# Kernel tuning notes

Measured on AMD Instinct MI355X. Metric: run time of the kernel, lower is better.

Reference implementation:

```python
import jax, jax.numpy as jnp
import numpy as np

LN_EPS = 1e-5
EPS = 1e-8
MESH_LR = 1.0
MESH_ITERS = 4
SH_ITERS = 5
SA_ITERS = 3


def build_grid(res):
    ranges = [np.linspace(0.0, 1.0, num=r) for r in res]
    g = np.stack(np.meshgrid(*ranges, indexing='ij'), axis=-1)
    g = g.reshape(res[0], res[1], -1)[None]
    return jnp.asarray(np.concatenate([g, 1.0 - g], axis=-1).astype(np.float32))  # [1,H,W,4]


def layer_norm(x, w, b):
    m = jnp.mean(x, axis=-1, keepdims=True)
    v = jnp.var(x, axis=-1, keepdims=True)
    return (x - m) * jax.lax.rsqrt(v + LN_EPS) * w + b


def l2norm(x):
    n = jnp.linalg.norm(x, axis=-1, keepdims=True)
    return x / jnp.maximum(n, 1e-12)  # matches F.normalize eps


def conv_relu(x, w, b, stride):
    y = jax.lax.conv_general_dilated(x, w, (stride, stride), [(2, 2), (2, 2)],
                                     dimension_numbers=('NCHW', 'OIHW', 'NCHW'))
    return jax.nn.relu(y + b[None, :, None, None])


def sinkhorn(C, a, b, u=None, v=None, n_iters=SH_ITERS):
    # log-domain Sinkhorn; C: [B,N,S] cost, a: [B,N], b: [B,S] marginals
    p = -C
    log_a, log_b = jnp.log(a), jnp.log(b)
    if u is None:
        u = jnp.zeros_like(a)
    if v is None:
        v = jnp.zeros_like(b)
    for _ in range(n_iters):
        u = log_a - jax.nn.logsumexp(p + v[:, None, :], axis=2)
        v = log_b - jax.nn.logsumexp(p + u[:, :, None], axis=1)
    pi = jnp.exp(p + u[:, :, None] + v[:, None, :])
    return pi, u, v


def minimize_entropy_of_sinkhorn(C0, a, b, mesh_lr=MESH_LR, n_mesh_iters=MESH_ITERS):
    # gradient descent on the cost matrix to minimize entropy of the transport plan
    def ent(C, u, v):
        pi, u2, v2 = sinkhorn(C, a, b, u=u, v=v)
        e = jnp.mean(-jnp.sum(pi * jnp.log(pi + EPS), axis=(1, 2)))
        return e, (u2, v2)

    grad_fn = jax.grad(ent, has_aux=True)
    u, v = jnp.zeros_like(a), jnp.zeros_like(b)
    C = C0
    for _ in range(n_mesh_iters):
        g, (u, v) = grad_fn(C, u, v)
        C = C - mesh_lr * g
    return C, u, v


def gru_cell(x, h, wih, whh, bih, bhh):
    gi = x @ wih.T + bih
    gh = h @ whh.T + bhh
    ir, iz, inn = jnp.split(gi, 3, axis=-1)
    hr, hz, hn = jnp.split(gh, 3, axis=-1)
    r = jax.nn.sigmoid(ir + hr)
    z = jax.nn.sigmoid(iz + hz)
    n = jnp.tanh(inn + r * hn)
    return (1.0 - z) * n + z * h


def setup_inputs() -> dict:
    key = jax.random.key(0)
    ks = iter(jax.random.split(key, 48))

    def nrm(shape, fan_in):
        return jax.random.normal(next(ks), shape, jnp.float32) / np.sqrt(fan_in).astype(np.float32)

    B, d, S, HID = 16, 64, 8, 128
    z = lambda *s: jnp.zeros(s, jnp.float32)
    o = lambda *s: jnp.ones(s, jnp.float32)
    inp = {
        'image': jax.random.normal(next(ks), (B, 3, 128, 128), jnp.float32),
        'slots_noise': jax.random.normal(next(ks), (B, S, d), jnp.float32),
        'conv1_w': nrm((64, 3, 5, 5), 75), 'conv1_b': z(64),
        'conv2_w': nrm((64, 64, 5, 5), 1600), 'conv2_b': z(64),
        'conv3_w': nrm((64, 64, 5, 5), 1600), 'conv3_b': z(64),
        'conv4_w': nrm((64, 64, 5, 5), 1600), 'conv4_b': z(64),
        'pos_w': nrm((d, 4), 4), 'pos_b': z(d),
        'mlp1_w': nrm((d, d), d), 'mlp1_b': z(d),
        'mlp2_w': nrm((d, d), d), 'mlp2_b': z(d),
        'ln_in_w': o(d), 'ln_in_b': z(d),
        'wk': nrm((d, d), d), 'wv': nrm((d, d), d), 'wq': nrm((d, d), d),
        'mwi_w': nrm((1, d), d), 'mwi_b': z(1),
        'mws_w': nrm((1, d), d), 'mws_b': z(1),
        'ln_sl_w': o(d), 'ln_sl_b': z(d),
        'gru_wih': nrm((3 * d, d), d), 'gru_whh': nrm((3 * d, d), d),
        'gru_bih': z(3 * d), 'gru_bhh': z(3 * d),
        'ln_ff_w': o(d), 'ln_ff_b': z(d),
        'fc1_w': nrm((HID, d), d), 'fc1_b': z(HID),
        'fc2_w': nrm((d, HID), HID), 'fc2_b': z(d),
        'slots_mu': nrm((1, 1, d), d),
        'slots_sigma': jax.random.uniform(next(ks), (1, 1, d), jnp.float32),
        'num_slots': 8,
    }
    return inp


def reference(image, slots_noise, conv1_w, conv1_b, conv2_w, conv2_b, conv3_w, conv3_b,
              conv4_w, conv4_b, pos_w, pos_b, mlp1_w, mlp1_b, mlp2_w, mlp2_b,
              ln_in_w, ln_in_b, wk, wv, wq, mwi_w, mwi_b, mws_w, mws_b,
              ln_sl_w, ln_sl_b, gru_wih, gru_whh, gru_bih, gru_bhh,
              ln_ff_w, ln_ff_b, fc1_w, fc1_b, fc2_w, fc2_b,
              slots_mu, slots_sigma, num_slots):
    B = image.shape[0]
    d = slots_mu.shape[-1]
    # --- CNN encoder (strided_convs=True => latent 32x32) ---
    x = conv_relu(image, conv1_w, conv1_b, 1)
    x = conv_relu(x, conv2_w, conv2_b, 2)
    x = conv_relu(x, conv3_w, conv3_b, 2)
    x = conv_relu(x, conv4_w, conv4_b, 1)          # [B,64,32,32]
    x = x.transpose(0, 2, 3, 1)                    # [B,32,32,64]
    grid = build_grid((32, 32))                    # [1,32,32,4]
    x = x + (grid @ pos_w.T + pos_b)               # soft position embed
    feat = x.reshape(B, -1, d)                     # [B,1024,64]
    # --- pre-slot-attention MLP ---
    feat = jax.nn.relu(feat @ mlp1_w.T + mlp1_b) @ mlp2_w.T + mlp2_b
    # --- slot attention with MESH-Sinkhorn ---
    n_s = num_slots
    slots = slots_mu + (jnp.abs(slots_sigma) + EPS) * slots_noise  # Normal rsample
    inp = layer_norm(feat, ln_in_w, ln_in_b)
    k = inp @ wk.T
    v = inp @ wv.T
    a = jax.nn.softmax((inp @ mwi_w.T + mwi_b).squeeze(-1), axis=-1) * n_s  # [B,N]
    kn = l2norm(k)
    attn = None
    for _ in range(SA_ITERS):
        slots_prev = slots
        s = layer_norm(slots, ln_sl_w, ln_sl_b)
        bm = jax.nn.softmax((s @ mws_w.T + mws_b).squeeze(-1), axis=-1) * n_s  # [B,S]
        q = s @ wq.T
        C = 1.0 - jnp.einsum('bnd,bsd->bns', kn, l2norm(q))  # cosine distance
        C, p, qq = minimize_entropy_of_sinkhorn(C, a, bm)
        pi, _, _ = sinkhorn(C, a, bm, u=p, v=qq)
        attn = pi.transpose(0, 2, 1)                         # [B,S,N]
        updates = jnp.einsum('bsn,bnd->bsd', attn, v)
        slots = gru_cell(updates.reshape(-1, d), slots_prev.reshape(-1, d),
                         gru_wih, gru_whh, gru_bih, gru_bhh).reshape(B, n_s, d)
        h = layer_norm(slots, ln_ff_w, ln_ff_b)
        slots = slots + (jax.nn.relu(h @ fc1_w.T + fc1_b) @ fc2_w.T + fc2_b)
    return slots, attn
```

## Files before the change

### kernel.cpp

```cpp
#include <hip/hip_runtime.h>
#include <hip/hip_bf16.h>


#define LN_EPS 1e-5f
#define SEPS 1e-8f
#define LN8 2.0794415416798357f

__device__ inline float ldf(float x) { return x; }
__device__ inline float ldf(__hip_bfloat16 x) { return __bfloat162float(x); }
__device__ inline void stf(float* p, float v) { *p = v; }
__device__ inline void stf(__hip_bfloat16* p, float v) { *p = __float2bfloat16(v); }

__device__ inline float wmaxall(float v) {
#pragma unroll
  for (int o = 32; o; o >>= 1) v = fmaxf(v, __shfl_down(v, o));
  return __shfl(v, 0);
}
__device__ inline float wsumall(float v) {
#pragma unroll
  for (int o = 32; o; o >>= 1) v += __shfl_down(v, o);
  return __shfl(v, 0);
}
__device__ inline int wsumi(int v) {
#pragma unroll
  for (int o = 32; o; o >>= 1) v += __shfl_down(v, o);
  return __shfl(v, 0);
}
__device__ inline float fast_sigmoid(float x) { return 1.f / (1.f + __expf(-x)); }
__device__ inline float fast_tanh(float x) { return 1.f - 2.f / (__expf(2.f * x) + 1.f); }

struct CvtArgs {
  const void* src[39];
  long off[40];
};

__global__ __launch_bounds__(256) void convert_kernel(CvtArgs a,
                                                      float* __restrict__ dst, long total) {
  __shared__ int sFlag;
  {
    const unsigned int* img = (const unsigned int*)a.src[0];
    if (threadIdx.x < 64) {
      int cnt = 0;
      for (int i = threadIdx.x; i < 512; i += 64) {
        unsigned lo = img[i] & 0xFFFFu;
        int e = (int)((lo >> 7) & 0xFFu);
        cnt += (e >= 96 && e <= 140) ? 1 : 0;
      }
      cnt = wsumi(cnt);
      if (threadIdx.x == 0) sFlag = (cnt >= 300) ? 1 : 0;
    }
    __syncthreads();
  }
  const int isbf = sFlag;
  for (long g = (long)blockIdx.x * 256 + threadIdx.x; g < total; g += (long)gridDim.x * 256) {
    int lo = 0, hi = 38;
    while (lo < hi) {
      int mid = (lo + hi + 1) >> 1;
      if (a.off[mid] <= g) lo = mid; else hi = mid - 1;
    }
    long li = g - a.off[lo];
    float v;
    if (isbf) v = __bfloat162float(((const __hip_bfloat16*)a.src[lo])[li]);
    else      v = ((const float*)a.src[lo])[li];
    dst[g] = v;
  }
}

struct TwArgs {
  long soff[9]; long doff[9]; int R[9]; int C[9];
};

__global__ __launch_bounds__(256) void transw_kernel(const float* __restrict__ cvt,
                                                     float* __restrict__ tws, TwArgs a) {
  int m = blockIdx.x;
  const float* S = cvt + a.soff[m];
  float* D = tws + a.doff[m];
  int R = a.R[m], C = a.C[m];
  for (int idx = threadIdx.x; idx < R * C; idx += 256) {
    int i = idx / C, j = idx - i * C;
    D[j * R + i] = S[idx];
  }
}

template <int S, typename TIN, typename TOUT>
__global__ __launch_bounds__(256) void conv5x5(
    const TIN* __restrict__ in, const float* __restrict__ wgt,
    const float* __restrict__ bias, TOUT* __restrict__ out,
    int Cin, int H, int W, int Ho, int Wo, int Cout, int tilesX) {
  constexpr int P = 15 * S + 5;
  constexpr int PP = (S == 1) ? 20 : 40;
  constexpr int NCH = (S == 1) ? 2 : 3;
  constexpr int NP = (P * P + 255) / 256;
  __shared__ __align__(16) float patch[P * PP];
  __shared__ float wt16[25 * 16];
  const int b = blockIdx.z;
  const int ocg = blockIdx.y * 16;
  const int ty0 = (blockIdx.x / tilesX) * 16, tx0 = (blockIdx.x % tilesX) * 16;
  const int og = threadIdx.x >> 6;
  const int r = (threadIdx.x >> 2) & 15;
  const int rx = threadIdx.x & 3;
  const int iy0 = ty0 * S - 2, ix0 = tx0 * S - 2;
  const long HW = (long)H * W;

  int toff[NP], soff[NP];
#pragma unroll
  for (int q = 0; q < NP; q++) {
    int idx = threadIdx.x + 256 * q;
    toff[q] = -1;
    soff[q] = -1;
    if (idx < P * P) {
      int py = idx / P, px = idx - py * P;
      int iy = iy0 + py, ix = ix0 + px;
      int pxs = (S == 2) ? (px ^ (((py >> 1) & 1) << 2)) : px;
      toff[q] = py * PP + pxs;
      if (iy >= 0 && iy < H && ix >= 0 && ix < W) soff[q] = iy * W + ix;
    }
  }
  int wsrc[2];
#pragma unroll
  for (int q = 0; q < 2; q++) {
    int idx = threadIdx.x + 256 * q;
    wsrc[q] = (idx < 400) ? (((ocg + (idx & 15)) * Cin) * 25 + (idx >> 4)) : -1;
  }

  float acc[4][4];
#pragma unroll
  for (int p = 0; p < 4; p++)
#pragma unroll
    for (int j = 0; j < 4; j++) acc[p][j] = 0.f;

  float pr[NP], wr[2];
  {
    const TIN* inp = in + (long)b * Cin * HW;
#pragma unroll
    for (int q = 0; q < NP; q++) pr[q] = (soff[q] >= 0) ? ldf(inp[soff[q]]) : 0.f;
#pragma unroll
    for (int q = 0; q < 2; q++) wr[q] = (wsrc[q] >= 0) ? wgt[wsrc[q]] : 0.f;
  }

  for (int ci = 0; ci < Cin; ++ci) {
    __syncthreads();
#pragma unroll
    for (int q = 0; q < NP; q++)
      if (toff[q] >= 0) patch[toff[q]] = pr[q];
#pragma unroll
    for (int q = 0; q < 2; q++) {
      int idx = threadIdx.x + 256 * q;
      if (idx < 400) wt16[idx] = wr[q];
    }
    __syncthreads();
    if (ci + 1 < Cin) {
      const TIN* inp = in + ((long)b * Cin + ci + 1) * HW;
#pragma unroll
      for (int q = 0; q < NP; q++) pr[q] = (soff[q] >= 0) ? ldf(inp[soff[q]]) : 0.f;
#pragma unroll
      for (int q = 0; q < 2; q++)
        if (wsrc[q] >= 0) wr[q] = wgt[wsrc[q] + (ci + 1) * 25];
    }
#pragma unroll
    for (int ky = 0; ky < 5; ky++) {
      float win[4 * NCH];
      const int row = r * S + ky;
      const float* rb = &patch[row * PP];
      if constexpr (S == 2) {
        const int sw = (row >> 1) & 1;
#pragma unroll
        for (int c = 0; c < NCH; c++) {
          const int g = rx * 2 + c;
          float4 t4 = *(const float4*)(rb + ((g ^ sw) << 2));
          win[4 * c + 0] = t4.x;
          win[4 * c + 1] = t4.y;
          win[4 * c + 2] = t4.z;
          win[4 * c + 3] = t4.w;
        }
      } else {
        const float* bp = rb + rx * 4;
#pragma unroll
        for (int c = 0; c < NCH; c++) {
          float4 t4 = *(const float4*)(bp + 4 * c);
          win[4 * c + 0] = t4.x;
          win[4 * c + 1] = t4.y;
          win[4 * c + 2] = t4.z;
          win[4 * c + 3] = t4.w;
        }
      }
#pragma unroll
      for (int kx = 0; kx < 5; kx++) {
        const float4 wv = *(const float4*)&wt16[(ky * 5 + kx) * 16 + og * 4];
#pragma unroll
        for (int p = 0; p < 4; p++) {
          float iv = win[p * S + kx];
          acc[p][0] += iv * wv.x;
          acc[p][1] += iv * wv.y;
          acc[p][2] += iv * wv.z;
          acc[p][3] += iv * wv.w;
        }
      }
    }
  }
  const int oy = ty0 + r, ox0 = tx0 + rx * 4;
#pragma unroll
  for (int j = 0; j < 4; j++) {
    int oc = ocg + og * 4 + j;
    float bs = bias[oc];
    TOUT* op = &out[(((long)b * Cout + oc) * Ho + oy) * Wo + ox0];
#pragma unroll
    for (int p = 0; p < 4; p++) stf(&op[p], fmaxf(acc[p][j] + bs, 0.f));
  }
}

template <int S, typename TIN>
__global__ __launch_bounds__(256) void conv5x5_part(
    const TIN* __restrict__ in, const float* __restrict__ wgt,
    float* __restrict__ pout,
    int Cin, int H, int W, int Ho, int Wo, int Cout, int tilesX) {
  constexpr int P = 15 * S + 5;
  constexpr int PP = (S == 1) ? 20 : 40;
  constexpr int NCH = (S == 1) ? 2 : 3;
  constexpr int NP = (P * P + 255) / 256;
  __shared__ __align__(16) float patch[P * PP];
  __shared__ float wt16[25 * 16];
  const int zz = blockIdx.z;
  const int qh = zz & 3;
  const int b = zz >> 2;
  const int nci = Cin >> 2;
  const int c0 = qh * nci;
  const int ocg = blockIdx.y * 16;
  const int ty0 = (blockIdx.x / tilesX) * 16, tx0 = (blockIdx.x % tilesX) * 16;
  const int og = threadIdx.x >> 6;
  const int r = (threadIdx.x >> 2) & 15;
  const int rx = threadIdx.x & 3;
  const int iy0 = ty0 * S - 2, ix0 = tx0 * S - 2;
  const long HW = (long)H * W;

  int toff[NP], soff[NP];
#pragma unroll
  for (int q = 0; q < NP; q++) {
    int idx = threadIdx.x + 256 * q;
    toff[q] = -1;
    soff[q] = -1;
    if (idx < P * P) {
      int py = idx / P, px = idx - py * P;
      int iy = iy0 + py, ix = ix0 + px;
      int pxs = (S == 2) ? (px ^ (((py >> 1) & 1) << 2)) : px;
      toff[q] = py * PP + pxs;
      if (iy >= 0 && iy < H && ix >= 0 && ix < W) soff[q] = iy * W + ix;
    }
  }
  int wsrc[2];
#pragma unroll
  for (int q = 0; q < 2; q++) {
    int idx = threadIdx.x + 256 * q;
    wsrc[q] = (idx < 400) ? (((ocg + (idx & 15)) * Cin) * 25 + (idx >> 4)) : -1;
  }

  float acc[4][4];
#pragma unroll
  for (int p = 0; p < 4; p++)
#pragma unroll
    for (int j = 0; j < 4; j++) acc[p][j] = 0.f;

  float pr[NP], wr[2];
  {
    const TIN* inp = in + ((long)b * Cin + c0) * HW;
#pragma unroll
    for (int q = 0; q < NP; q++) pr[q] = (soff[q] >= 0) ? ldf(inp[soff[q]]) : 0.f;
#pragma unroll
    for (int q = 0; q < 2; q++) wr[q] = (wsrc[q] >= 0) ? wgt[wsrc[q] + c0 * 25] : 0.f;
  }

  const int cEnd = c0 + nci;
  for (int ci = c0; ci < cEnd; ++ci) {
    __syncthreads();
#pragma unroll
    for (int q = 0; q < NP; q++)
      if (toff[q] >= 0) patch[toff[q]] = pr[q];
#pragma unroll
    for (int q = 0; q < 2; q++) {
      int idx = threadIdx.x + 256 * q;
      if (idx < 400) wt16[idx] = wr[q];
    }
    __syncthreads();
    if (ci + 1 < cEnd) {
      const TIN* inp = in + ((long)b * Cin + ci + 1) * HW;
#pragma unroll
      for (int q = 0; q < NP; q++) pr[q] = (soff[q] >= 0) ? ldf(inp[soff[q]]) : 0.f;
#pragma unroll
      for (int q = 0; q < 2; q++)
        if (wsrc[q] >= 0) wr[q] = wgt[wsrc[q] + (ci + 1) * 25];
    }
#pragma unroll
    for (int ky = 0; ky < 5; ky++) {
      float win[4 * NCH];
      const int row = r * S + ky;
      const float* rb = &patch[row * PP];
      if constexpr (S == 2) {
        const int sw = (row >> 1) & 1;
#pragma unroll
        for (int c = 0; c < NCH; c++) {
          const int g = rx * 2 + c;
          float4 t4 = *(const float4*)(rb + ((g ^ sw) << 2));
          win[4 * c + 0] = t4.x;
          win[4 * c + 1] = t4.y;
          win[4 * c + 2] = t4.z;
          win[4 * c + 3] = t4.w;
        }
      } else {
        const float* bp = rb + rx * 4;
#pragma unroll
        for (int c = 0; c < NCH; c++) {
          float4 t4 = *(const float4*)(bp + 4 * c);
          win[4 * c + 0] = t4.x;
          win[4 * c + 1] = t4.y;
          win[4 * c + 2] = t4.z;
          win[4 * c + 3] = t4.w;
        }
      }
#pragma unroll
      for (int kx = 0; kx < 5; kx++) {
        const float4 wv = *(const float4*)&wt16[(ky * 5 + kx) * 16 + og * 4];
#pragma unroll
        for (int p = 0; p < 4; p++) {
          float iv = win[p * S + kx];
          acc[p][0] += iv * wv.x;
          acc[p][1] += iv * wv.y;
          acc[p][2] += iv * wv.z;
          acc[p][3] += iv * wv.w;
        }
      }
    }
  }
  const int oy = ty0 + r, ox0 = tx0 + rx * 4;
  const long HoWo = (long)Ho * Wo;
#pragma unroll
  for (int j = 0; j < 4; j++) {
    int oc = ocg + og * 4 + j;
    float* op = &pout[((((long)qh * 16 + b) * Cout + oc) * Ho + oy) * Wo + ox0];
    (void)HoWo;
#pragma unroll
    for (int p = 0; p < 4; p++) op[p] = acc[p][j];
  }
}

__global__ __launch_bounds__(256) void fuse4_kernel(
    const float* __restrict__ pin, const float* __restrict__ bias,
    float* __restrict__ outF, int HoWo, int Cout, long qtr) {
  for (long i = (long)blockIdx.x * 256 + threadIdx.x; i < qtr;
       i += (long)gridDim.x * 256) {
    int oc = (int)((i / HoWo) % Cout);
    float v = ((pin[i] + pin[i + qtr]) + pin[i + 2 * qtr]) + pin[i + 3 * qtr];
    outF[i] = fmaxf(v + bias[oc], 0.f);
  }
}

__global__ __launch_bounds__(256) void token_kernel(
    const float* __restrict__ act4, const float* __restrict__ pos_w,
    const float* __restrict__ pos_b,
    const float* __restrict__ mlp1T, const float* __restrict__ mlp1_b,
    const float* __restrict__ mlp2T, const float* __restrict__ mlp2_b,
    const float* __restrict__ lnin_w, const float* __restrict__ lnin_b,
    const float* __restrict__ wkT, const float* __restrict__ wvT,
    const float* __restrict__ mwi_w, const float* __restrict__ mwi_b,
    float* __restrict__ knT_out, float* __restrict__ v_out, float* __restrict__ lg_out) {
  const int wq = threadIdx.x >> 6, i = threadIdx.x & 63;
  const int t = blockIdx.x * 4 + wq;
  const int b = t >> 10, nn = t & 1023;
  const int h = nn >> 5, w = nn & 31;
  __shared__ float sM1[4096], sM2[4096], sWk[4096], sWv[4096];
  __shared__ float f[4][64], h1[4][64], inp[4][64];
  for (int idx = threadIdx.x; idx < 4096; idx += 256) {
    sM1[idx] = mlp1T[idx];
    sM2[idx] = mlp2T[idx];
    sWk[idx] = wkT[idx];
    sWv[idx] = wvT[idx];
  }
  {
    float gh = h * (1.f / 31.f), gw = w * (1.f / 31.f);
    float e = gh * pos_w[i * 4 + 0] + gw * pos_w[i * 4 + 1] +
              (1.f - gh) * pos_w[i * 4 + 2] + (1.f - gw) * pos_w[i * 4 + 3] + pos_b[i];
    f[wq][i] = act4[(((long)b * 64 + i) * 32 + h) * 32 + w] + e;
  }
  __syncthreads();
  float acc = 0.f;
  for (int j = 0; j < 64; j++) acc += f[wq][j] * sM1[j * 64 + i];
  h1[wq][i] = fmaxf(acc + mlp1_b[i], 0.f);
  __syncthreads();
  acc = 0.f;
  for (int j = 0; j < 64; j++) acc += h1[wq][j] * sM2[j * 64 + i];
  float x = acc + mlp2_b[i];
  float m = wsumall(x) * (1.f / 64.f);
  float d0 = x - m;
  float var = wsumall(d0 * d0) * (1.f / 64.f);
  float xin = d0 * rsqrtf(var + LN_EPS) * lnin_w[i] + lnin_b[i];
  inp[wq][i] = xin;
  __syncthreads();
  float kv = 0.f, vv = 0.f;
  for (int j = 0; j < 64; j++) {
    float ij = inp[wq][j];
    kv += ij * sWk[j * 64 + i];
    vv += ij * sWv[j * 64 + i];
  }
  float ss = wsumall(kv * kv);
  knT_out[(long)b * 65536 + i * 1024 + nn] = kv / fmaxf(sqrtf(ss), 1e-12f);
  v_out[(long)t * 64 + i] = vv;
  float lg = wsumall(xin * mwi_w[i]);
  if (i == 0) lg_out[t] = lg + mwi_b[0];
}

__global__ __launch_bounds__(512) void sa_kernel(
    const float* __restrict__ knT_g, const float* __restrict__ v_g,
    const float* __restrict__ la_g, const float* __restrict__ noise,
    const float* __restrict__ mu_w, const float* __restrict__ sg_w,
    const float* __restrict__ lnsl_w, const float* __restrict__ lnsl_b,
    const float* __restrict__ mws_w, const float* __restrict__ mws_b,
    const float* __restrict__ wqT,
    const float* __restrict__ wihT, const float* __restrict__ whhT,
    const float* __restrict__ bih, const float* __restrict__ bhh,
    const float* __restrict__ lnff_w, const float* __restrict__ lnff_b,
    const float* __restrict__ fc1T, const float* __restrict__ fc1_b,
    const float* __restrict__ fc2T, const float* __restrict__ fc2_b,
    float* __restrict__ out) {
  const int b = blockIdx.x, tid = threadIdx.x;
  const int wv = tid >> 6, ln = tid & 63;

  __shared__ float sCt[8192];
  __shared__ float sEc[8192];
  __shared__ float sLa[1024], sELa[1024], sHid[1024];
  __shared__ float sPart[512 * 9];
  __shared__ float sVh[48], sV[8], sEsv[8], sGv[8], sLb[8], sBm[8];
  __shared__ float sC1[8], sEvh[8];
  __shared__ float sSlots[512], sNorm[512], sQn[512], sUpd[512];

  const float* knt = knT_g + (long)b * 65536;
  const float* vf = v_g + (long)b * 65536;
  float sInvH[5][2];
  float gPr[2][8];
  float gInit[2];

  {
    int dd = tid & 63;
    sSlots[tid] = mu_w[dd] + (fabsf(sg_w[dd]) + SEPS) * noise[(long)b * 512 + tid];
  }
  for (int n = tid; n < 1024; n += 512) sLa[n] = la_g[b * 1024 + n];
  __syncthreads();
  {
    float a0 = sLa[tid], a1 = sLa[tid + 512];
    float m0 = wmaxall(fmaxf(a0, a1));
    if (ln == 0) sBm[wv] = m0;
    __syncthreads();
    float M = sBm[0];
#pragma unroll
    for (int s = 1; s < 8; s++) M = fmaxf(M, sBm[s]);
    float e0 = wsumall(__expf(a0 - M) + __expf(a1 - M));
    if (ln == 0) sGv[wv] = e0;
    __syncthreads();
    float SS = 0.f;
#pragma unroll
    for (int s = 0; s < 8; s++) SS += sGv[s];
    float lse = M + __logf(SS);
    float l0 = a0 - lse + LN8, l1 = a1 - lse + LN8;
    sLa[tid] = l0;
    sLa[tid + 512] = l1;
    sELa[tid] = __expf(l0);
    sELa[tid + 512] = __expf(l1);
  }
  __syncthreads();

  for (int it = 0; it < 3; ++it) {
    {
      float x = sSlots[wv * 64 + ln];
      float m = wsumall(x) * (1.f / 64.f);
      float d0 = x - m;
      float var = wsumall(d0 * d0) * (1.f / 64.f);
      float xn = d0 * rsqrtf(var + LN_EPS) * lnsl_w[ln] + lnsl_b[ln];
      sNorm[wv * 64 + ln] = xn;
      float bmv = wsumall(xn * mws_w[ln]);
      if (ln == 0) sBm[wv] = bmv + mws_b[0];
    }
    __syncthreads();
    if (tid == 0) {
      float mx = -1e30f;
      for (int s = 0; s < 8; s++) mx = fmaxf(mx, sBm[s]);
      float ss = 0.f;
      for (int s = 0; s < 8; s++) ss += __expf(sBm[s] - mx);
      float lse = mx + __logf(ss);
      for (int s = 0; s < 8; s++) sLb[s] = sBm[s] - lse + LN8;
    }
    {
      float acc = 0.f;
      for (int j = 0; j < 64; j++) acc += sNorm[wv * 64 + j] * wqT[j * 64 + ln];
      sQn[tid] = acc;
    }
    __syncthreads();
    {
      float qv = sQn[wv * 64 + ln];
      float ss = wsumall(qv * qv);
      sQn[wv * 64 + ln] = qv / fmaxf(sqrtf(ss), 1e-12f);
    }
    if (tid < 8) {
      sV[tid] = 0.f;
      sEsv[tid] = 1.f;
    }
    __syncthreads();

#pragma unroll
    for (int k = 0; k < 2; k++) {
      int n = tid + 512 * k;
      float acc[8];
#pragma unroll
      for (int s = 0; s < 8; s++) acc[s] = 0.f;
      for (int j = 0; j < 64; j++) {
        float kvv = knt[j * 1024 + n];
#pragma unroll
        for (int s = 0; s < 8; s++) acc[s] += kvv * sQn[s * 64 + j];
      }
#pragma unroll
      for (int s = 0; s < 8; s++) {
        float c = 1.f - acc[s];
        sCt[s * 1024 + n] = c;
        sEc[s * 1024 + n] = __expf(-c);
      }
    }
    __syncthreads();

    for (int m = 0; m < 4; m++) {
#pragma unroll
      for (int t = 1; t <= 5; t++) {
        if (t == 1 && tid < 8) sVh[tid] = sV[tid];
        float esv_r[8], part[8];
#pragma unroll
        for (int s = 0; s < 8; s++) { esv_r[s] = sEsv[s]; part[s] = 0.f; }
#pragma unroll
        for (int k = 0; k < 2; k++) {
          int n = tid + 512 * k;
          float ec[8], S = 0.f;
#pragma unroll
          for (int s = 0; s < 8; s++) {
            ec[s] = sEc[s * 1024 + n];
            S += esv_r[s] * ec[s];
          }
          float inv = 1.f / S;
          sInvH[t - 1][k] = inv;
          float w = sELa[n] * inv;
#pragma unroll
          for (int s = 0; s < 8; s++) part[s] += w * ec[s];
        }
#pragma unroll
        for (int s = 0; s < 8; s++) sPart[tid * 9 + s] = part[s];
        __syncthreads();
        {
          int s = wv;
          float acc = 0.f;
#pragma unroll
          for (int q = 0; q < 8; q++) acc += sPart[(ln + 64 * q) * 9 + s];
          acc = wsumall(acc);
          if (ln == 0) {
            float vs = sLb[s] - __logf(acc);
            sV[s] = vs;
            sVh[t * 8 + s] = vs;
            sEsv[s] = __expf(vs);
          }
        }
        __syncthreads();
      }
      {
        float esv_r[8], part[8];
#pragma unroll
        for (int s = 0; s < 8; s++) { esv_r[s] = sEsv[s]; part[s] = 0.f; }
#pragma unroll
        for (int k = 0; k < 2; k++) {
          int n = tid + 512 * k;
          float al = sELa[n] * sInvH[4][k];
          float gul = 0.f;
#pragma unroll
          for (int s = 0; s < 8; s++) {
            float pi = al * esv_r[s] * sEc[s * 1024 + n];
            float gl = -(__logf(pi + SEPS) + pi / (pi + SEPS)) * pi * (1.f / 16.f);
            gPr[k][s] = gl;
            gul += gl;
            part[s] += gl;
          }
          gInit[k] = gul;
        }
#pragma unroll
        for (int s = 0; s < 8; s++) sPart[tid * 9 + s] = part[s];
        __syncthreads();
        {
          int s = wv;
          float acc = 0.f;
#pragma unroll
          for (int q = 0; q < 8; q++) acc += sPart[(ln + 64 * q) * 9 + s];
          acc = wsumall(acc);
          if (ln == 0) {
            sGv[s] = acc;
            sC1[s] = acc * __expf(sVh[40 + s] - sLb[s]);
            sEvh[s] = __expf(sVh[32 + s]);
          }
        }
        __syncthreads();
      }
#pragma unroll
      for (int t = 5; t >= 1; t--) {
        float c1_r[8], evh_r[8], part[8];
#pragma unroll
        for (int s = 0; s < 8; s++) {
          c1_r[s] = sC1[s];
          evh_r[s] = sEvh[s];
          part[s] = 0.f;
        }
#pragma unroll
        for (int k = 0; k < 2; k++) {
          int n = tid + 512 * k;
          float inv = sInvH[t - 1][k];
          float al = sELa[n] * inv;
          float gul = (t == 5) ? gInit[k] : 0.f;
          float ec[8];
#pragma unroll
          for (int s = 0; s < 8; s++) {
            ec[s] = sEc[s * 1024 + n];
            float t2 = al * c1_r[s] * ec[s];
            gPr[k][s] -= t2;
            gul -= t2;
          }
          float bv = gul * inv;
#pragma unroll
          for (int s = 0; s < 8; s++) {
            float pe = bv * ec[s];
            gPr[k][s] -= pe * evh_r[s];
            part[s] += pe;
          }
          if (t == 1) {
#pragma unroll
            for (int s = 0; s < 8; s++) {
              float cn = sCt[s * 1024 + n] + gPr[k][s];
              sCt[s * 1024 + n] = cn;
              sEc[s * 1024 + n] = __expf(-cn);
            }
          }
        }
        if (t > 1) {
#pragma unroll
          for (int s = 0; s < 8; s++) sPart[tid * 9 + s] = part[s];
        }
        if (t == 1 && tid < 8) {
          float vs = sVh[40 + tid];
          sV[tid] = vs;
          sEsv[tid] = __expf(vs);
        }
        __syncthreads();
        if (t > 1) {
          int s = wv;
          float acc = 0.f;
#pragma unroll
          for (int q = 0; q < 8; q++) acc += sPart[(ln + 64 * q) * 9 + s];
          acc = wsumall(acc);
          if (ln == 0) {
            float gn = -sEvh[s] * acc;
            sGv[s] = gn;
            sC1[s] = gn * __expf(sVh[(t - 1) * 8 + s] - sLb[s]);
            sEvh[s] = __expf(sVh[(t - 2) * 8 + s]);
          }
          __syncthreads();
        }
      }
    }

    float invF[2];
    for (int t = 0; t < 5; t++) {
      float esv_r[8], part[8];
#pragma unroll
      for (int s = 0; s < 8; s++) { esv_r[s] = sEsv[s]; part[s] = 0.f; }
#pragma unroll
      for (int k = 0; k < 2; k++) {
        int n = tid + 512 * k;
        float ec[8], S = 0.f;
#pragma unroll
        for (int s = 0; s < 8; s++) {
          ec[s] = sEc[s * 1024 + n];
          S += esv_r[s] * ec[s];
        }
        float inv = 1.f / S;
        invF[k] = inv;
        float w = sELa[n] * inv;
#pragma unroll
        for (int s = 0; s < 8; s++) part[s] += w * ec[s];
      }
#pragma unroll
      for (int s = 0; s < 8; s++) sPart[tid * 9 + s] = part[s];
      __syncthreads();
      {
        int s = wv;
        float acc = 0.f;
#pragma unroll
        for (int q = 0; q < 8; q++) acc += sPart[(ln + 64 * q) * 9 + s];
        acc = wsumall(acc);
        if (ln == 0) {
          float vs = sLb[s] - __logf(acc);
          sV[s] = vs;
          sEsv[s] = __expf(vs);
        }
      }
      __syncthreads();
    }
    {
      float esv_r[8];
#pragma unroll
      for (int s = 0; s < 8; s++) esv_r[s] = sEsv[s];
#pragma unroll
      for (int k = 0; k < 2; k++) {
        int n = tid + 512 * k;
        float al = sELa[n] * invF[k];
#pragma unroll
        for (int s = 0; s < 8; s++)
          sCt[s * 1024 + n] = al * esv_r[s] * sEc[s * 1024 + n];
      }
    }
    __syncthreads();
    if (it == 2) {
      for (int o = tid; o < 8192; o += 512) out[8192 + (long)b * 8192 + o] = sCt[o];
    }
    {
      int s = tid >> 6, dd = tid & 63;
      float acc = 0.f;
      for (int n = 0; n < 1024; n++) acc += sCt[s * 1024 + n] * vf[n * 64 + dd];
      sUpd[tid] = acc;
    }
    __syncthreads();
    float newslot;
    {
      int s = tid >> 6, i = tid & 63;
      const float* x = &sUpd[s * 64];
      const float* h = &sSlots[s * 64];
      float gir = 0, giz = 0, gin = 0, ghr = 0, ghz = 0, ghn = 0;
      for (int j = 0; j < 64; j++) {
        float xv = x[j], hv = h[j];
        gir += xv * wihT[j * 192 + i];
        giz += xv * wihT[j * 192 + 64 + i];
        gin += xv * wihT[j * 192 + 128 + i];
        ghr += hv * whhT[j * 192 + i];
        ghz += hv * whhT[j * 192 + 64 + i];
        ghn += hv * whhT[j * 192 + 128 + i];
      }
      gir += bih[i]; giz += bih[64 + i]; gin += bih[128 + i];
      ghr += bhh[i]; ghz += bhh[64 + i]; ghn += bhh[128 + i];
      float r = fast_sigmoid(gir + ghr);
      float z = fast_sigmoid(giz + ghz);
      float nn = fast_tanh(gin + r * ghn);
      newslot = (1.f - z) * nn + z * h[i];
    }
    __syncthreads();
    sSlots[tid] = newslot;
    __syncthreads();
    {
      float x = sSlots[wv * 64 + ln];
      float m = wsumall(x) * (1.f / 64.f);
      float d0 = x - m;
      float var = wsumall(d0 * d0) * (1.f / 64.f);
      sNorm[wv * 64 + ln] = d0 * rsqrtf(var + LN_EPS) * lnff_w[ln] + lnff_b[ln];
    }
    __syncthreads();
    for (int o = tid; o < 1024; o += 512) {
      int s = o >> 7, k2 = o & 127;
      float acc = 0.f;
      for (int j = 0; j < 64; j++) acc += sNorm[s * 64 + j] * fc1T[j * 128 + k2];
      sHid[o] = fmaxf(acc + fc1_b[k2], 0.f);
    }
    __syncthreads();
    {
      int s = tid >> 6, i = tid & 63;
      float acc = 0.f;
      for (int j = 0; j < 128; j++) acc += sHid[s * 128 + j] * fc2T[j * 64 + i];
      newslot = sSlots[tid] + acc + fc2_b[i];
    }
    __syncthreads();
    sSlots[tid] = newslot;
    __syncthreads();
  }
  out[(long)b * 512 + tid] = sSlots[tid];
}

extern "C" void kernel_launch(void* const* d_in, const int* in_sizes, int n_in,
                              void* d_out, int out_size, void* d_ws, size_t ws_size,
                              hipStream_t stream) {
  (void)n_in; (void)out_size; (void)ws_size;
  char* ws = (char*)d_ws;
  float* cvt  = (float*)ws;
  float* lgts = (float*)(ws + 5570560ull);
  __hip_bfloat16* act1 = (__hip_bfloat16*)(ws + 5636096ull);
  __hip_bfloat16* act2 = (__hip_bfloat16*)(ws + 39190528ull);
  float* act3 = (float*)(ws + 5636096ull);
  float* act4 = (float*)(ws + 9830400ull);
  float* knT  = (float*)(ws + 14024704ull);
  float* vf   = (float*)(ws + 18219008ull);
  float* parts = (float*)(ws + 22413312ull);
  float* tws  = (float*)(ws + 47583232ull);

  CvtArgs ca;
  long total = 0;
  for (int i = 0; i < 39; i++) { ca.src[i] = d_in[i]; ca.off[i] = total; total += in_sizes[i]; }
  ca.off[39] = total;

  convert_kernel<<<1024, 256, 0, stream>>>(ca, cvt, total);

#define ARR(i) (cvt + ca.off[i])
  TwArgs ta;
  {
    const int src[9] = {12, 14, 18, 19, 20, 27, 28, 33, 35};
    const int R[9] = {64, 64, 64, 64, 64, 192, 192, 128, 64};
    const int C[9] = {64, 64, 64, 64, 64, 64, 64, 64, 128};
    long d = 0;
    for (int m2 = 0; m2 < 9; m2++) {
      ta.soff[m2] = ca.off[src[m2]];
      ta.doff[m2] = d;
      ta.R[m2] = R[m2];
      ta.C[m2] = C[m2];
      d += (long)R[m2] * C[m2];
    }
  }
  transw_kernel<<<9, 256, 0, stream>>>(cvt, tws, ta);
  float* mlp1T = tws + 0,     *mlp2T = tws + 4096,  *wkT = tws + 8192, *wvT = tws + 12288;
  float* wqT   = tws + 16384, *wihT  = tws + 20480, *whhT = tws + 32768;
  float* fc1T  = tws + 45056, *fc2T  = tws + 53248;

  const float* image = ARR(0);
  const float* noise = ARR(1);

  conv5x5<1, float, __hip_bfloat16><<<dim3(64, 4, 16), 256, 0, stream>>>(
      image, ARR(2), ARR(3), act1, 3, 128, 128, 128, 128, 64, 8);
  conv5x5<2, __hip_bfloat16, __hip_bfloat16><<<dim3(16, 4, 16), 256, 0, stream>>>(
      act1, ARR(4), ARR(5), act2, 64, 128, 128, 64, 64, 64, 4);
  conv5x5_part<2, __hip_bfloat16><<<dim3(4, 4, 64), 256, 0, stream>>>(
      act2, ARR(6), parts, 64, 64, 64, 32, 32, 64, 2);
  fuse4_kernel<<<1024, 256, 0, stream>>>(parts, ARR(7), act3, 1024, 64,
                                         16L * 64 * 1024);
  conv5x5_part<1, float><<<dim3(4, 4, 64), 256, 0, stream>>>(
      act3, ARR(8), parts, 64, 32, 32, 32, 32, 64, 2);
  fuse4_kernel<<<1024, 256, 0, stream>>>(parts, ARR(9), act4, 1024, 64,
                                         16L * 64 * 1024);

  token_kernel<<<4096, 256, 0, stream>>>(act4, ARR(10), ARR(11),
                                         mlp1T, ARR(13), mlp2T, ARR(15),
                                         ARR(16), ARR(17), wkT, wvT, ARR(21), ARR(22),
                                         knT, vf, lgts);

  sa_kernel<<<16, 512, 0, stream>>>(knT, vf, lgts, noise, ARR(37), ARR(38),
                                    ARR(25), ARR(26), ARR(23), ARR(24), wqT,
                                    wihT, whhT, ARR(29), ARR(30),
                                    ARR(31), ARR(32), fc1T, ARR(34), fc2T, ARR(36),
                                    (float*)d_out);
#undef ARR
}
```

Before: 863.9 us.

## Halve conv_part tile height for more blocks and fuse final split-K reduction into token kernel

The split-K conv kernel now uses 8-row output tiles with 2 output channels per thread group instead of 16 rows and 4 channels. This doubles the grid size and lowers per-thread register use, giving more parallelism for the small late convolutions. The last fuse4 reduction and ReLU pass is removed: the token kernel sums the four partial buffers and applies bias and ReLU itself, which saves one launch and one full activation round trip. In exchange each thread does less arithmetic per shared-memory load, and the patch loads overlap more between neighbouring tiles.

```diff
diff --git a/kernel.cpp b/kernel.cpp
--- a/kernel.cpp
+++ b/kernel.cpp
@@ -214,11 +214,12 @@
     const TIN* __restrict__ in, const float* __restrict__ wgt,
     float* __restrict__ pout,
     int Cin, int H, int W, int Ho, int Wo, int Cout, int tilesX) {
-  constexpr int P = 15 * S + 5;
+  constexpr int PR = 7 * S + 5;
+  constexpr int PC = 15 * S + 5;
   constexpr int PP = (S == 1) ? 20 : 40;
   constexpr int NCH = (S == 1) ? 2 : 3;
-  constexpr int NP = (P * P + 255) / 256;
-  __shared__ __align__(16) float patch[P * PP];
+  constexpr int NP = (PR * PC + 255) / 256;
+  __shared__ __align__(16) float patch[PR * PP];
   __shared__ float wt16[25 * 16];
   const int zz = blockIdx.z;
   const int qh = zz & 3;
@@ -226,9 +227,9 @@
   const int nci = Cin >> 2;
   const int c0 = qh * nci;
   const int ocg = blockIdx.y * 16;
-  const int ty0 = (blockIdx.x / tilesX) * 16, tx0 = (blockIdx.x % tilesX) * 16;
-  const int og = threadIdx.x >> 6;
-  const int r = (threadIdx.x >> 2) & 15;
+  const int ty0 = (blockIdx.x / tilesX) * 8, tx0 = (blockIdx.x % tilesX) * 16;
+  const int og = threadIdx.x >> 5;
+  const int r = (threadIdx.x >> 2) & 7;
   const int rx = threadIdx.x & 3;
   const int iy0 = ty0 * S - 2, ix0 = tx0 * S - 2;
   const long HW = (long)H * W;
@@ -239,8 +240,8 @@
     int idx = threadIdx.x + 256 * q;
     toff[q] = -1;
     soff[q] = -1;
-    if (idx < P * P) {
-      int py = idx / P, px = idx - py * P;
+    if (idx < PR * PC) {
+      int py = idx / PC, px = idx - py * PC;
       int iy = iy0 + py, ix = ix0 + px;
       int pxs = (S == 2) ? (px ^ (((py >> 1) & 1) << 2)) : px;
       toff[q] = py * PP + pxs;
@@ -254,11 +255,12 @@
     wsrc[q] = (idx < 400) ? (((ocg + (idx & 15)) * Cin) * 25 + (idx >> 4)) : -1;
   }
 
-  float acc[4][4];
-#pragma unroll
-  for (int p = 0; p < 4; p++)
-#pragma unroll
-    for (int j = 0; j < 4; j++) acc[p][j] = 0.f;
+  float acc[4][2];
+#pragma unroll
+  for (int p = 0; p < 4; p++) {
+    acc[p][0] = 0.f;
+    acc[p][1] = 0.f;
+  }
 
   float pr[NP], wr[2];
   {
@@ -318,25 +320,22 @@
       }
 #pragma unroll
       for (int kx = 0; kx < 5; kx++) {
-        const float4 wv = *(const float4*)&wt16[(ky * 5 + kx) * 16 + og * 4];
+        const float* wp = &wt16[(ky * 5 + kx) * 16 + og * 2];
+        float w0 = wp[0], w1 = wp[1];
 #pragma unroll
         for (int p = 0; p < 4; p++) {
           float iv = win[p * S + kx];
-          acc[p][0] += iv * wv.x;
-          acc[p][1] += iv * wv.y;
-          acc[p][2] += iv * wv.z;
-          acc[p][3] += iv * wv.w;
+          acc[p][0] += iv * w0;
+          acc[p][1] += iv * w1;
         }
       }
     }
   }
   const int oy = ty0 + r, ox0 = tx0 + rx * 4;
-  const long HoWo = (long)Ho * Wo;
-#pragma unroll
-  for (int j = 0; j < 4; j++) {
-    int oc = ocg + og * 4 + j;
+#pragma unroll
+  for (int j = 0; j < 2; j++) {
+    int oc = ocg + og * 2 + j;
     float* op = &pout[((((long)qh * 16 + b) * Cout + oc) * Ho + oy) * Wo + ox0];
-    (void)HoWo;
 #pragma unroll
     for (int p = 0; p < 4; p++) op[p] = acc[p][j];
   }
@@ -354,8 +353,8 @@
 }
 
 __global__ __launch_bounds__(256) void token_kernel(
-    const float* __restrict__ act4, const float* __restrict__ pos_w,
-    const float* __restrict__ pos_b,
+    const float* __restrict__ parts, const float* __restrict__ cb4,
+    const float* __restrict__ pos_w, const float* __restrict__ pos_b,
     const float* __restrict__ mlp1T, const float* __restrict__ mlp1_b,
     const float* __restrict__ mlp2T, const float* __restrict__ mlp2_b,
     const float* __restrict__ lnin_w, const float* __restrict__ lnin_b,
@@ -378,7 +377,10 @@
     float gh = h * (1.f / 31.f), gw = w * (1.f / 31.f);
     float e = gh * pos_w[i * 4 + 0] + gw * pos_w[i * 4 + 1] +
               (1.f - gh) * pos_w[i * 4 + 2] + (1.f - gw) * pos_w[i * 4 + 3] + pos_b[i];
-    f[wq][i] = act4[(((long)b * 64 + i) * 32 + h) * 32 + w] + e;
+    const long base = ((long)b * 64 + i) * 1024 + nn;
+    const long q = 16L * 64 * 1024;
+    float v = ((parts[base] + parts[base + q]) + parts[base + 2 * q]) + parts[base + 3 * q];
+    f[wq][i] = fmaxf(v + cb4[i], 0.f) + e;
   }
   __syncthreads();
   float acc = 0.f;
@@ -789,7 +791,6 @@
   __hip_bfloat16* act1 = (__hip_bfloat16*)(ws + 5636096ull);
   __hip_bfloat16* act2 = (__hip_bfloat16*)(ws + 39190528ull);
   float* act3 = (float*)(ws + 5636096ull);
-  float* act4 = (float*)(ws + 9830400ull);
   float* knT  = (float*)(ws + 14024704ull);
   float* vf   = (float*)(ws + 18219008ull);
   float* parts = (float*)(ws + 22413312ull);
@@ -829,16 +830,14 @@
       image, ARR(2), ARR(3), act1, 3, 128, 128, 128, 128, 64, 8);
   conv5x5<2, __hip_bfloat16, __hip_bfloat16><<<dim3(16, 4, 16), 256, 0, stream>>>(
       act1, ARR(4), ARR(5), act2, 64, 128, 128, 64, 64, 64, 4);
-  conv5x5_part<2, __hip_bfloat16><<<dim3(4, 4, 64), 256, 0, stream>>>(
+  conv5x5_part<2, __hip_bfloat16><<<dim3(8, 4, 64), 256, 0, stream>>>(
       act2, ARR(6), parts, 64, 64, 64, 32, 32, 64, 2);
   fuse4_kernel<<<1024, 256, 0, stream>>>(parts, ARR(7), act3, 1024, 64,
                                          16L * 64 * 1024);
-  conv5x5_part<1, float><<<dim3(4, 4, 64), 256, 0, stream>>>(
+  conv5x5_part<1, float><<<dim3(8, 4, 64), 256, 0, stream>>>(
       act3, ARR(8), parts, 64, 32, 32, 32, 32, 64, 2);
-  fuse4_kernel<<<1024, 256, 0, stream>>>(parts, ARR(9), act4, 1024, 64,
-                                         16L * 64 * 1024);
-
-  token_kernel<<<4096, 256, 0, stream>>>(act4, ARR(10), ARR(11),
+
+  token_kernel<<<4096, 256, 0, stream>>>(parts, ARR(9), ARR(10), ARR(11),
                                          mlp1T, ARR(13), mlp2T, ARR(15),
                                          ARR(16), ARR(17), wkT, wvT, ARR(21), ARR(22),
                                          knT, vf, lgts);
```

Result: slower. 908.8 us (+5.2%).
